# Optimization experiments

Measured on AMD Instinct MI355X. Metric: run time of the kernel, lower is better.

## Reference

```python
import jax, jax.numpy as jnp
import numpy as np

B, N, K, C = 2, 2048, 48, 128
FF = 4 * C
EPS = 1e-5
SCALE = 30.0

def _gelu(x):
    return jax.nn.gelu(x, approximate=False)

def _ln(x, g, b):
    m = jnp.mean(x, axis=-1, keepdims=True)
    v = jnp.var(x, axis=-1, keepdims=True)
    return g * (x - m) * jax.lax.rsqrt(v + EPS) + b

def _gather_nodes(nodes, idx):
    # nodes [B,N,C], idx [B,N,K] -> [B,N,K,C]
    return jnp.take_along_axis(nodes[:, :, None, :], idx[..., None], axis=1)

def setup_inputs() -> dict:
    key = jax.random.key(0)
    ks = jax.random.split(key, 16)
    def w(k, i, o):
        return (jax.random.normal(k, (i, o), jnp.float32) / np.sqrt(i)).astype(jnp.float32)
    inp = {
        'h_V': jax.random.normal(ks[0], (B, N, C), jnp.float32),
        'h_E': jax.random.normal(ks[1], (B, N, K, C), jnp.float32),
        'E_idx': jax.random.randint(ks[2], (B, N, K), 0, N),
        'mask_V': jnp.ones((B, N), jnp.float32),
        'mask_attend': jnp.ones((B, N, K), jnp.float32),
        'W1_w': w(ks[3], 3 * C, C), 'W1_b': jnp.zeros((C,), jnp.float32),
        'W2_w': w(ks[4], C, C), 'W2_b': jnp.zeros((C,), jnp.float32),
        'W3_w': w(ks[5], C, C), 'W3_b': jnp.zeros((C,), jnp.float32),
        'W11_w': w(ks[6], 3 * C, C), 'W11_b': jnp.zeros((C,), jnp.float32),
        'W12_w': w(ks[7], C, C), 'W12_b': jnp.zeros((C,), jnp.float32),
        'W13_w': w(ks[8], C, C), 'W13_b': jnp.zeros((C,), jnp.float32),
        'Win_w': w(ks[9], C, FF), 'Win_b': jnp.zeros((FF,), jnp.float32),
        'Wout_w': w(ks[10], FF, C), 'Wout_b': jnp.zeros((C,), jnp.float32),
        'g1': jnp.ones((C,), jnp.float32), 'b1': jnp.zeros((C,), jnp.float32),
        'g2': jnp.ones((C,), jnp.float32), 'b2': jnp.zeros((C,), jnp.float32),
        'g3': jnp.ones((C,), jnp.float32), 'b3': jnp.zeros((C,), jnp.float32),
    }
    return inp

def _edge_mlp(h_V, h_E, E_idx, Wa_w, Wa_b, Wb_w, Wb_b, Wc_w, Wc_b):
    h_nbr = _gather_nodes(h_V, E_idx)                       # [B,N,K,C]
    h_ctr = jnp.broadcast_to(h_V[:, :, None, :], h_nbr.shape)
    h_EV = jnp.concatenate([h_ctr, h_E, h_nbr], axis=-1)   # [B,N,K,3C]
    h = _gelu(h_EV @ Wa_w + Wa_b)
    h = _gelu(h @ Wb_w + Wb_b)
    return h @ Wc_w + Wc_b                                  # [B,N,K,C]

def reference(h_V, h_E, E_idx, mask_V, mask_attend,
              W1_w, W1_b, W2_w, W2_b, W3_w, W3_b,
              W11_w, W11_b, W12_w, W12_b, W13_w, W13_b,
              Win_w, Win_b, Wout_w, Wout_b,
              g1, b1, g2, b2, g3, b3):
    # message pass on nodes
    h_msg = _edge_mlp(h_V, h_E, E_idx, W1_w, W1_b, W2_w, W2_b, W3_w, W3_b)
    h_msg = mask_attend[..., None] * h_msg
    dh = jnp.sum(h_msg, axis=-2) / SCALE
    h_V = _ln(h_V + dh, g1, b1)
    # position-wise FFN
    dh = _gelu(h_V @ Win_w + Win_b) @ Wout_w + Wout_b
    h_V = _ln(h_V + dh, g2, b2)
    h_V = mask_V[..., None] * h_V
    # edge update
    h_msg = _edge_mlp(h_V, h_E, E_idx, W11_w, W11_b, W12_w, W12_b, W13_w, W13_b)
    h_E = _ln(h_E + h_msg, g3, b3)
    return (h_V, h_E)
```

## Files before the change

### kernel.cpp

```cpp
#include <hip/hip_runtime.h>
#include <hip/hip_bf16.h>

#define BB 2
#define NN 2048
#define KE 48
#define CC 128
#define FFD 512
#define K3 384

typedef short sx8 __attribute__((ext_vector_type(8)));
typedef float fx4 __attribute__((ext_vector_type(4)));

__device__ __forceinline__ short f2bs(float f) {
    __bf16 h = (__bf16)f;
    return __builtin_bit_cast(short, h);
}

__device__ __forceinline__ float gelu_f(float x) {
    float z = fabsf(x) * 0.70710678118654752f;
    float e = __expf(-z * z);
    float t = __builtin_amdgcn_rcpf(fmaf(0.3275911f, z, 1.0f));
    float poly = t * fmaf(t, fmaf(t, fmaf(t, fmaf(t, 1.061405429f, -1.453152027f),
                                          1.421413741f), -0.284496736f), 0.254829592f);
    float erf = 1.0f - poly * e;
    float phi = fmaf(copysignf(erf, x), 0.5f, 0.5f);
    return x * phi;
}

__device__ __forceinline__ sx8 cvt8f(const float* p) {
    float4 a = *(const float4*)p;
    float4 b = *(const float4*)(p + 4);
    sx8 r;
    r[0] = f2bs(a.x); r[1] = f2bs(a.y); r[2] = f2bs(a.z); r[3] = f2bs(a.w);
    r[4] = f2bs(b.x); r[5] = f2bs(b.y); r[6] = f2bs(b.z); r[7] = f2bs(b.w);
    return r;
}

__device__ __forceinline__ sx8 pack8(float4 a, float4 b) {
    sx8 r;
    r[0] = f2bs(a.x); r[1] = f2bs(a.y); r[2] = f2bs(a.z); r[3] = f2bs(a.w);
    r[4] = f2bs(b.x); r[5] = f2bs(b.y); r[6] = f2bs(b.z); r[7] = f2bs(b.w);
    return r;
}

__global__ void prep_weights(const float* __restrict__ W1, const float* __restrict__ W2,
                             const float* __restrict__ W3, const float* __restrict__ W11,
                             const float* __restrict__ W12, const float* __restrict__ W13,
                             const float* __restrict__ Win, const float* __restrict__ Wout,
                             short* __restrict__ wt) {
    int i = blockIdx.x * 256 + threadIdx.x;
    const float* src;
    short* dst;
    int R, S, local;
    if (i < 49152)       { src = W1;   dst = wt;          R = 384; S = 128; local = i; }
    else if (i < 65536)  { src = W2;   dst = wt + 49152;  R = 128; S = 128; local = i - 49152; }
    else if (i < 81920)  { src = W3;   dst = wt + 65536;  R = 128; S = 128; local = i - 65536; }
    else if (i < 131072) { src = W11;  dst = wt + 81920;  R = 384; S = 128; local = i - 81920; }
    else if (i < 147456) { src = W12;  dst = wt + 131072; R = 128; S = 128; local = i - 131072; }
    else if (i < 163840) { src = W13;  dst = wt + 147456; R = 128; S = 128; local = i - 147456; }
    else if (i < 229376) { src = Win;  dst = wt + 163840; R = 128; S = 512; local = i - 163840; }
    else                 { src = Wout; dst = wt + 229376; R = 512; S = 128; local = i - 229376; }
    int c = local / R;
    int r = local - c * R;
    dst[local] = f2bs(src[r * S + c]);
}

template <int PASS>
__global__ __launch_bounds__(256, 5) void edge_pass(
    const float* __restrict__ hVsrc, const float* __restrict__ hE,
    const int* __restrict__ Eidx,
    const short* __restrict__ WaT, const float* __restrict__ Wab,
    const short* __restrict__ WbT, const float* __restrict__ Wbb,
    const short* __restrict__ WcT, const float* __restrict__ Wcb,
    const float* __restrict__ mask_att, float* __restrict__ hv1_out,
    const float* __restrict__ gamma, const float* __restrict__ beta,
    float* __restrict__ hE_out) {
    __shared__ __align__(16) unsigned char smem_raw[48 * 264 * 2];

    short* A0   = (short*)smem_raw;
    short* Xs   = (short*)smem_raw;
    float* S    = (float*)smem_raw;
    float* dhp  = (float*)(smem_raw + 13056);
    float* redp = (float*)(smem_raw + 15104);

    const int tid = threadIdx.x;
    const int bn  = blockIdx.x;
    const int bb  = bn >> 11;
    const int wave = tid >> 6, lane = tid & 63, q = lane >> 4, m16 = lane & 15;
    const int col0 = wave * 32 + m16;
    const int col1 = col0 + 16;
    const int r0 = tid >> 4, seg = tid & 15;

    const int e0 = Eidx[bn * KE + r0];
    const int e1 = Eidx[bn * KE + r0 + 16];
    const int e2 = Eidx[bn * KE + r0 + 32];

    {
        const float* he  = hE + (size_t)bn * KE * CC + seg * 8;
        float4 h0a = *(const float4*)(he + r0 * CC);
        float4 h0b = *(const float4*)(he + r0 * CC + 4);
        float4 h1a = *(const float4*)(he + (r0 + 16) * CC);
        float4 h1b = *(const float4*)(he + (r0 + 16) * CC + 4);
        float4 h2a = *(const float4*)(he + (r0 + 32) * CC);
        float4 h2b = *(const float4*)(he + (r0 + 32) * CC + 4);
        *(sx8*)(A0 + r0 * 264 + seg * 8)        = pack8(h0a, h0b);
        *(sx8*)(A0 + (r0 + 16) * 264 + seg * 8) = pack8(h1a, h1b);
        *(sx8*)(A0 + (r0 + 32) * 264 + seg * 8) = pack8(h2a, h2b);
    }
    {
        const float* hvb = hVsrc + (size_t)bb * NN * CC + seg * 8;
        float4 n0a = *(const float4*)(hvb + (size_t)e0 * CC);
        float4 n0b = *(const float4*)(hvb + (size_t)e0 * CC + 4);
        float4 n1a = *(const float4*)(hvb + (size_t)e1 * CC);
        float4 n1b = *(const float4*)(hvb + (size_t)e1 * CC + 4);
        float4 n2a = *(const float4*)(hvb + (size_t)e2 * CC);
        float4 n2b = *(const float4*)(hvb + (size_t)e2 * CC + 4);
        *(sx8*)(A0 + r0 * 264 + 128 + seg * 8)        = pack8(n0a, n0b);
        *(sx8*)(A0 + (r0 + 16) * 264 + 128 + seg * 8) = pack8(n1a, n1b);
        *(sx8*)(A0 + (r0 + 32) * 264 + 128 + seg * 8) = pack8(n2a, n2b);
    }

    const float* ctr = hVsrc + (size_t)bn * CC;
    fx4 acc[3][2];
    {
        sx8 cA[4], s0f[4], s1f[4];
#pragma unroll
        for (int kk = 0; kk < 4; ++kk) {
            cA[kk]  = cvt8f(ctr + kk * 32 + q * 8);
            s0f[kk] = *(const sx8*)(WaT + col0 * K3 + kk * 32 + q * 8);
            s1f[kk] = *(const sx8*)(WaT + col1 * K3 + kk * 32 + q * 8);
        }
        fx4 c0, c1;
#pragma unroll
        for (int r = 0; r < 4; ++r) { c0[r] = 0.0f; c1[r] = 0.0f; }
#pragma unroll
        for (int kk = 0; kk < 4; ++kk) {
            c0 = __builtin_amdgcn_mfma_f32_16x16x32_bf16(cA[kk], s0f[kk], c0, 0, 0, 0);
            c1 = __builtin_amdgcn_mfma_f32_16x16x32_bf16(cA[kk], s1f[kk], c1, 0, 0, 0);
        }
#pragma unroll
        for (int mt = 0; mt < 3; ++mt) { acc[mt][0] = c0; acc[mt][1] = c1; }
    }

    sx8 b0[4], b1[4];
#pragma unroll
    for (int kk = 0; kk < 4; ++kk) {
        b0[kk] = *(const sx8*)(WaT + col0 * K3 + 128 + kk * 32 + q * 8);
        b1[kk] = *(const sx8*)(WaT + col1 * K3 + 128 + kk * 32 + q * 8);
    }
    __syncthreads();

#pragma unroll
    for (int half = 0; half < 2; ++half) {
        if (half) {
#pragma unroll
            for (int kk = 0; kk < 4; ++kk) {
                b0[kk] = *(const sx8*)(WaT + col0 * K3 + 256 + kk * 32 + q * 8);
                b1[kk] = *(const sx8*)(WaT + col1 * K3 + 256 + kk * 32 + q * 8);
            }
        }
#pragma unroll
        for (int kk = 0; kk < 4; ++kk) {
#pragma unroll
            for (int mt = 0; mt < 3; ++mt) {
                sx8 af = *(const sx8*)(A0 + (mt * 16 + m16) * 264 + half * 128 + kk * 32 + q * 8);
                acc[mt][0] = __builtin_amdgcn_mfma_f32_16x16x32_bf16(af, b0[kk], acc[mt][0], 0, 0, 0);
                acc[mt][1] = __builtin_amdgcn_mfma_f32_16x16x32_bf16(af, b1[kk], acc[mt][1], 0, 0, 0);
            }
        }
    }

    sx8 p0[4], p1[4];
#pragma unroll
    for (int kk = 0; kk < 4; ++kk) {
        p0[kk] = *(const sx8*)(WbT + col0 * CC + kk * 32 + q * 8);
        p1[kk] = *(const sx8*)(WbT + col1 * CC + kk * 32 + q * 8);
    }
    __syncthreads();

    {
        float ba0 = Wab[col0], ba1 = Wab[col1];
#pragma unroll
        for (int mt = 0; mt < 3; ++mt)
#pragma unroll
            for (int r = 0; r < 4; ++r) {
                int row = mt * 16 + q * 4 + r;
                Xs[row * 136 + col0] = f2bs(gelu_f(acc[mt][0][r] + ba0));
                Xs[row * 136 + col1] = f2bs(gelu_f(acc[mt][1][r] + ba1));
            }
    }
    __syncthreads();

    fx4 acc2[3][2];
#pragma unroll
    for (int mt = 0; mt < 3; ++mt)
#pragma unroll
        for (int nt = 0; nt < 2; ++nt)
#pragma unroll
            for (int r = 0; r < 4; ++r) acc2[mt][nt][r] = 0.0f;
#pragma unroll
    for (int kk = 0; kk < 4; ++kk) {
#pragma unroll
        for (int mt = 0; mt < 3; ++mt) {
            sx8 af = *(const sx8*)(Xs + (mt * 16 + m16) * 136 + kk * 32 + q * 8);
            acc2[mt][0] = __builtin_amdgcn_mfma_f32_16x16x32_bf16(af, p0[kk], acc2[mt][0], 0, 0, 0);
            acc2[mt][1] = __builtin_amdgcn_mfma_f32_16x16x32_bf16(af, p1[kk], acc2[mt][1], 0, 0, 0);
        }
    }

    sx8 t0[4], t1[4];
#pragma unroll
    for (int kk = 0; kk < 4; ++kk) {
        t0[kk] = *(const sx8*)(WcT + col0 * CC + kk * 32 + q * 8);
        t1[kk] = *(const sx8*)(WcT + col1 * CC + kk * 32 + q * 8);
    }
    float mrow[12];
    float res0[12], res1[12];
    if constexpr (PASS == 1) {
#pragma unroll
        for (int mt = 0; mt < 3; ++mt)
#pragma unroll
            for (int r = 0; r < 4; ++r)
                mrow[mt * 4 + r] = mask_att[bn * KE + mt * 16 + q * 4 + r];
    } else {
#pragma unroll
        for (int mt = 0; mt < 3; ++mt)
#pragma unroll
            for (int r = 0; r < 4; ++r) {
                int row = mt * 16 + q * 4 + r;
                res0[mt * 4 + r] = hE[((size_t)bn * KE + row) * CC + col0];
                res1[mt * 4 + r] = hE[((size_t)bn * KE + row) * CC + col1];
            }
    }
    __syncthreads();

    {
        float bb0 = Wbb[col0], bb1 = Wbb[col1];
#pragma unroll
        for (int mt = 0; mt < 3; ++mt)
#pragma unroll
            for (int r = 0; r < 4; ++r) {
                int row = mt * 16 + q * 4 + r;
                Xs[row * 136 + col0] = f2bs(gelu_f(acc2[mt][0][r] + bb0));
                Xs[row * 136 + col1] = f2bs(gelu_f(acc2[mt][1][r] + bb1));
            }
    }
    __syncthreads();

    fx4 acc3[3][2];
#pragma unroll
    for (int mt = 0; mt < 3; ++mt)
#pragma unroll
        for (int nt = 0; nt < 2; ++nt)
#pragma unroll
            for (int r = 0; r < 4; ++r) acc3[mt][nt][r] = 0.0f;
#pragma unroll
    for (int kk = 0; kk < 4; ++kk) {
#pragma unroll
        for (int mt = 0; mt < 3; ++mt) {
            sx8 af = *(const sx8*)(Xs + (mt * 16 + m16) * 136 + kk * 32 + q * 8);
            acc3[mt][0] = __builtin_amdgcn_mfma_f32_16x16x32_bf16(af, t0[kk], acc3[mt][0], 0, 0, 0);
            acc3[mt][1] = __builtin_amdgcn_mfma_f32_16x16x32_bf16(af, t1[kk], acc3[mt][1], 0, 0, 0);
        }
    }

    float bc0 = Wcb[col0], bc1 = Wcb[col1];

    if constexpr (PASS == 1) {
        float ps0 = 0.f, ps1 = 0.f;
#pragma unroll
        for (int mt = 0; mt < 3; ++mt)
#pragma unroll
            for (int r = 0; r < 4; ++r) {
                float m = mrow[mt * 4 + r];
                ps0 += m * (acc3[mt][0][r] + bc0);
                ps1 += m * (acc3[mt][1][r] + bc1);
            }
        dhp[q * 128 + col0] = ps0;
        dhp[q * 128 + col1] = ps1;
        __syncthreads();
        float val = 0.f;
        if (tid < 128) {
            float dh = dhp[tid] + dhp[128 + tid] + dhp[256 + tid] + dhp[384 + tid];
            val = hVsrc[(size_t)bn * CC + tid] + dh * (1.0f / 30.0f);
            float sv1 = val, sv2 = val * val;
#pragma unroll
            for (int m = 32; m >= 1; m >>= 1) {
                sv1 += __shfl_xor(sv1, m);
                sv2 += __shfl_xor(sv2, m);
            }
            if ((tid & 63) == 0) {
                redp[(tid >> 6) * 2]     = sv1;
                redp[(tid >> 6) * 2 + 1] = sv2;
            }
        }
        __syncthreads();
        if (tid < 128) {
            float mean = (redp[0] + redp[2]) * (1.0f / 128.0f);
            float var  = (redp[1] + redp[3]) * (1.0f / 128.0f) - mean * mean;
            float rstd = rsqrtf(fmaxf(var, 0.0f) + 1e-5f);
            hv1_out[(size_t)bn * CC + tid] = gamma[tid] * (val - mean) * rstd + beta[tid];
        }
    } else {
        __syncthreads();
#pragma unroll
        for (int mt = 0; mt < 3; ++mt)
#pragma unroll
            for (int r = 0; r < 4; ++r) {
                int row = mt * 16 + q * 4 + r;
                S[row * 132 + col0] = res0[mt * 4 + r] + acc3[mt][0][r] + bc0;
                S[row * 132 + col1] = res1[mt * 4 + r] + acc3[mt][1][r] + bc1;
            }
        __syncthreads();
        int g = tid >> 5, l32 = tid & 31;
        for (int r = g; r < 48; r += 8) {
            float x0 = S[r * 132 + l32];
            float x1 = S[r * 132 + l32 + 32];
            float x2 = S[r * 132 + l32 + 64];
            float x3 = S[r * 132 + l32 + 96];
            float sv1 = x0 + x1 + x2 + x3;
            float sv2 = x0 * x0 + x1 * x1 + x2 * x2 + x3 * x3;
#pragma unroll
            for (int m = 16; m >= 1; m >>= 1) {
                sv1 += __shfl_xor(sv1, m, 32);
                sv2 += __shfl_xor(sv2, m, 32);
            }
            float mean = sv1 * (1.0f / 128.0f);
            float var  = sv2 * (1.0f / 128.0f) - mean * mean;
            float rstd = rsqrtf(fmaxf(var, 0.0f) + 1e-5f);
            float* orow = hE_out + ((size_t)bn * KE + r) * CC;
            orow[l32]      = gamma[l32] * (x0 - mean) * rstd + beta[l32];
            orow[l32 + 32] = gamma[l32 + 32] * (x1 - mean) * rstd + beta[l32 + 32];
            orow[l32 + 64] = gamma[l32 + 64] * (x2 - mean) * rstd + beta[l32 + 64];
            orow[l32 + 96] = gamma[l32 + 96] * (x3 - mean) * rstd + beta[l32 + 96];
        }
    }
}

__global__ __launch_bounds__(256, 1) void ffn_kernel(
    float* __restrict__ hv, const short* __restrict__ WinT,
    const float* __restrict__ Winb, const short* __restrict__ WoutT,
    const float* __restrict__ Woutb, const float* __restrict__ g2,
    const float* __restrict__ b2, const float* __restrict__ maskV) {
    __shared__ __align__(16) float hvF[16 * 132];
    __shared__ __align__(16) short Abf[16 * 136];
    __shared__ __align__(16) short Xs[16 * 520];

    const int tid = threadIdx.x;
    const int bn  = blockIdx.x;
    const int wave = tid >> 6, lane = tid & 63, q = lane >> 4, m16 = lane & 15;
    const int col0 = wave * 32 + m16, col1 = col0 + 16;

    sx8 bw[4][8];
#pragma unroll
    for (int kk = 0; kk < 4; ++kk)
#pragma unroll
        for (int nt = 0; nt < 8; ++nt)
            bw[kk][nt] = *(const sx8*)(WinT + (wave * 128 + nt * 16 + m16) * CC + kk * 32 + q * 8);

    for (int i = tid; i < 512; i += 256) {
        int row = i >> 5;
        int c4  = (i & 31) * 4;
        float4 v = *(const float4*)(hv + (bn * 16 + row) * CC + c4);
        hvF[row * 132 + c4]     = v.x;
        hvF[row * 132 + c4 + 1] = v.y;
        hvF[row * 132 + c4 + 2] = v.z;
        hvF[row * 132 + c4 + 3] = v.w;
        Abf[row * 136 + c4]     = f2bs(v.x);
        Abf[row * 136 + c4 + 1] = f2bs(v.y);
        Abf[row * 136 + c4 + 2] = f2bs(v.z);
        Abf[row * 136 + c4 + 3] = f2bs(v.w);
    }
    __syncthreads();

    fx4 acc1[8];
#pragma unroll
    for (int nt = 0; nt < 8; ++nt)
#pragma unroll
        for (int r = 0; r < 4; ++r) acc1[nt][r] = 0.0f;

#pragma unroll
    for (int kk = 0; kk < 4; ++kk) {
        sx8 af = *(const sx8*)(Abf + m16 * 136 + kk * 32 + q * 8);
#pragma unroll
        for (int nt = 0; nt < 8; ++nt)
            acc1[nt] = __builtin_amdgcn_mfma_f32_16x16x32_bf16(af, bw[kk][nt], acc1[nt], 0, 0, 0);
    }

    sx8 c0a[16], c1a[16];
#pragma unroll
    for (int kk = 0; kk < 16; ++kk) {
        c0a[kk] = *(const sx8*)(WoutT + col0 * FFD + kk * 32 + q * 8);
        c1a[kk] = *(const sx8*)(WoutT + col1 * FFD + kk * 32 + q * 8);
    }

#pragma unroll
    for (int nt = 0; nt < 8; ++nt) {
        int coln = wave * 128 + nt * 16 + m16;
        float bi = Winb[coln];
#pragma unroll
        for (int r = 0; r < 4; ++r) {
            int row = q * 4 + r;
            Xs[row * 520 + coln] = f2bs(gelu_f(acc1[nt][r] + bi));
        }
    }
    __syncthreads();

    fx4 o0, o1;
#pragma unroll
    for (int r = 0; r < 4; ++r) { o0[r] = 0.0f; o1[r] = 0.0f; }
#pragma unroll
    for (int kk = 0; kk < 16; ++kk) {
        sx8 af = *(const sx8*)(Xs + m16 * 520 + kk * 32 + q * 8);
        o0 = __builtin_amdgcn_mfma_f32_16x16x32_bf16(af, c0a[kk], o0, 0, 0, 0);
        o1 = __builtin_amdgcn_mfma_f32_16x16x32_bf16(af, c1a[kk], o1, 0, 0, 0);
    }
    {
        float bo0 = Woutb[col0], bo1 = Woutb[col1];
#pragma unroll
        for (int r = 0; r < 4; ++r) {
            int row = q * 4 + r;
            hvF[row * 132 + col0] += o0[r] + bo0;
            hvF[row * 132 + col1] += o1[r] + bo1;
        }
    }
    __syncthreads();

    int g = tid >> 5, l32 = tid & 31;
#pragma unroll
    for (int rr = 0; rr < 2; ++rr) {
        int row = g + rr * 8;
        float x0 = hvF[row * 132 + l32];
        float x1 = hvF[row * 132 + l32 + 32];
        float x2 = hvF[row * 132 + l32 + 64];
        float x3 = hvF[row * 132 + l32 + 96];
        float s1 = x0 + x1 + x2 + x3;
        float s2 = x0 * x0 + x1 * x1 + x2 * x2 + x3 * x3;
#pragma unroll
        for (int m = 16; m >= 1; m >>= 1) {
            s1 += __shfl_xor(s1, m, 32);
            s2 += __shfl_xor(s2, m, 32);
        }
        float mean = s1 * (1.0f / 128.0f);
        float var  = s2 * (1.0f / 128.0f) - mean * mean;
        float rstd = rsqrtf(fmaxf(var, 0.0f) + 1e-5f);
        int node = bn * 16 + row;
        float mk = maskV[node];
        float* orow = hv + node * CC;
        orow[l32]      = mk * (g2[l32] * (x0 - mean) * rstd + b2[l32]);
        orow[l32 + 32] = mk * (g2[l32 + 32] * (x1 - mean) * rstd + b2[l32 + 32]);
        orow[l32 + 64] = mk * (g2[l32 + 64] * (x2 - mean) * rstd + b2[l32 + 64]);
        orow[l32 + 96] = mk * (g2[l32 + 96] * (x3 - mean) * rstd + b2[l32 + 96]);
    }
}

extern "C" void kernel_launch(void* const* d_in, const int* in_sizes, int n_in,
                              void* d_out, int out_size, void* d_ws, size_t ws_size,
                              hipStream_t stream) {
    (void)in_sizes; (void)n_in; (void)out_size; (void)ws_size;
    const float* hV    = (const float*)d_in[0];
    const float* hE    = (const float*)d_in[1];
    const int*   Eidx  = (const int*)d_in[2];
    const float* maskV = (const float*)d_in[3];
    const float* maskA = (const float*)d_in[4];
    const float* W1w  = (const float*)d_in[5];
    const float* W1b  = (const float*)d_in[6];
    const float* W2w  = (const float*)d_in[7];
    const float* W2b  = (const float*)d_in[8];
    const float* W3w  = (const float*)d_in[9];
    const float* W3b  = (const float*)d_in[10];
    const float* W11w = (const float*)d_in[11];
    const float* W11b = (const float*)d_in[12];
    const float* W12w = (const float*)d_in[13];
    const float* W12b = (const float*)d_in[14];
    const float* W13w = (const float*)d_in[15];
    const float* W13b = (const float*)d_in[16];
    const float* Winw = (const float*)d_in[17];
    const float* Winb = (const float*)d_in[18];
    const float* Woutw = (const float*)d_in[19];
    const float* Woutb = (const float*)d_in[20];
    const float* g1 = (const float*)d_in[21];
    const float* b1 = (const float*)d_in[22];
    const float* g2 = (const float*)d_in[23];
    const float* b2 = (const float*)d_in[24];
    const float* g3 = (const float*)d_in[25];
    const float* b3 = (const float*)d_in[26];

    short* wt   = (short*)d_ws;
    float* outV = (float*)d_out;
    float* outE = outV + (size_t)BB * NN * CC;

    prep_weights<<<1152, 256, 0, stream>>>(W1w, W2w, W3w, W11w, W12w, W13w, Winw, Woutw, wt);
    edge_pass<1><<<BB * NN, 256, 0, stream>>>(hV, hE, Eidx,
                                              wt, W1b, wt + 49152, W2b, wt + 65536, W3b,
                                              maskA, outV, g1, b1, nullptr);
    ffn_kernel<<<256, 256, 0, stream>>>(outV, wt + 163840, Winb, wt + 229376, Woutb, g2, b2, maskV);
    edge_pass<2><<<BB * NN, 256, 0, stream>>>(outV, hE, Eidx,
                                              wt + 81920, W11b, wt + 131072, W12b, wt + 147456, W13b,
                                              nullptr, nullptr, g3, b3, outE);
}
```

Measured before the change: 395.0 us.

## Precompute per-node center and neighbor projections of first edge layer

The first edge-MLP layer is split by linearity. The center and neighbor parts of W·[h_ctr,h_E,h_nbr] are computed once per node in a new precompute kernel, yielding Pc and Pn. The edge kernel then gathers the Pn rows for each neighbor and only runs the h_E third of the matmul, which cuts first-layer MFMA work to a third and shrinks shared memory. The cost is two extra launches, an fp32 scratch buffer, and scattered per-element gathers of Pn in place of coalesced row loads.

```diff
diff --git a/kernel.cpp b/kernel.cpp
--- a/kernel.cpp
+++ b/kernel.cpp
@@ -65,17 +65,61 @@
     dst[local] = f2bs(src[r * S + c]);
 }
 
+__global__ __launch_bounds__(256) void precompute_P(
+    const float* __restrict__ hv, const short* __restrict__ WT,
+    const float* __restrict__ bias, float* __restrict__ Pc,
+    float* __restrict__ Pn) {
+    __shared__ __align__(16) short Abf[16 * 136];
+    const int tid = threadIdx.x;
+    const int bn  = blockIdx.x;
+    const int wave = tid >> 6, lane = tid & 63, q = lane >> 4, m16 = lane & 15;
+    const int col0 = wave * 32 + m16, col1 = col0 + 16;
+
+    {
+        int row = tid >> 4, seg = tid & 15;
+        Abf[row * 136 + seg * 8 + 0] = 0;
+        *(sx8*)(Abf + row * 136 + seg * 8) = cvt8f(hv + (size_t)(bn * 16 + row) * CC + seg * 8);
+    }
+    __syncthreads();
+
+    fx4 c0, c1, n0, n1;
+#pragma unroll
+    for (int r = 0; r < 4; ++r) { c0[r] = 0.f; c1[r] = 0.f; n0[r] = 0.f; n1[r] = 0.f; }
+#pragma unroll
+    for (int kk = 0; kk < 4; ++kk) {
+        sx8 af = *(const sx8*)(Abf + m16 * 136 + kk * 32 + q * 8);
+        sx8 bc0 = *(const sx8*)(WT + col0 * K3 + kk * 32 + q * 8);
+        sx8 bc1 = *(const sx8*)(WT + col1 * K3 + kk * 32 + q * 8);
+        sx8 bn0 = *(const sx8*)(WT + col0 * K3 + 256 + kk * 32 + q * 8);
+        sx8 bn1 = *(const sx8*)(WT + col1 * K3 + 256 + kk * 32 + q * 8);
+        c0 = __builtin_amdgcn_mfma_f32_16x16x32_bf16(af, bc0, c0, 0, 0, 0);
+        c1 = __builtin_amdgcn_mfma_f32_16x16x32_bf16(af, bc1, c1, 0, 0, 0);
+        n0 = __builtin_amdgcn_mfma_f32_16x16x32_bf16(af, bn0, n0, 0, 0, 0);
+        n1 = __builtin_amdgcn_mfma_f32_16x16x32_bf16(af, bn1, n1, 0, 0, 0);
+    }
+    float bi0 = bias[col0], bi1 = bias[col1];
+#pragma unroll
+    for (int r = 0; r < 4; ++r) {
+        int node = bn * 16 + q * 4 + r;
+        Pc[(size_t)node * CC + col0] = c0[r] + bi0;
+        Pc[(size_t)node * CC + col1] = c1[r] + bi1;
+        Pn[(size_t)node * CC + col0] = n0[r];
+        Pn[(size_t)node * CC + col1] = n1[r];
+    }
+}
+
 template <int PASS>
 __global__ __launch_bounds__(256, 5) void edge_pass(
     const float* __restrict__ hVsrc, const float* __restrict__ hE,
     const int* __restrict__ Eidx,
-    const short* __restrict__ WaT, const float* __restrict__ Wab,
+    const short* __restrict__ WaT,
     const short* __restrict__ WbT, const float* __restrict__ Wbb,
     const short* __restrict__ WcT, const float* __restrict__ Wcb,
+    const float* __restrict__ Pc, const float* __restrict__ Pn,
     const float* __restrict__ mask_att, float* __restrict__ hv1_out,
     const float* __restrict__ gamma, const float* __restrict__ beta,
     float* __restrict__ hE_out) {
-    __shared__ __align__(16) unsigned char smem_raw[48 * 264 * 2];
+    __shared__ __align__(16) unsigned char smem_raw[PASS == 1 ? 15120 : 25344];
 
     short* A0   = (short*)smem_raw;
     short* Xs   = (short*)smem_raw;
@@ -91,55 +135,36 @@
     const int col1 = col0 + 16;
     const int r0 = tid >> 4, seg = tid & 15;
 
-    const int e0 = Eidx[bn * KE + r0];
-    const int e1 = Eidx[bn * KE + r0 + 16];
-    const int e2 = Eidx[bn * KE + r0 + 32];
+    int e[3][4];
+#pragma unroll
+    for (int mt = 0; mt < 3; ++mt)
+#pragma unroll
+        for (int r = 0; r < 4; ++r)
+            e[mt][r] = Eidx[bn * KE + mt * 16 + q * 4 + r];
+
+    float pc0 = Pc[(size_t)bn * CC + col0];
+    float pc1 = Pc[(size_t)bn * CC + col1];
+    float pn0[3][4], pn1[3][4];
+#pragma unroll
+    for (int mt = 0; mt < 3; ++mt)
+#pragma unroll
+        for (int r = 0; r < 4; ++r) {
+            size_t prow = ((size_t)bb * NN + e[mt][r]) * CC;
+            pn0[mt][r] = Pn[prow + col0];
+            pn1[mt][r] = Pn[prow + col1];
+        }
 
     {
-        const float* he  = hE + (size_t)bn * KE * CC + seg * 8;
+        const float* he = hE + (size_t)bn * KE * CC + seg * 8;
         float4 h0a = *(const float4*)(he + r0 * CC);
         float4 h0b = *(const float4*)(he + r0 * CC + 4);
         float4 h1a = *(const float4*)(he + (r0 + 16) * CC);
         float4 h1b = *(const float4*)(he + (r0 + 16) * CC + 4);
         float4 h2a = *(const float4*)(he + (r0 + 32) * CC);
         float4 h2b = *(const float4*)(he + (r0 + 32) * CC + 4);
-        *(sx8*)(A0 + r0 * 264 + seg * 8)        = pack8(h0a, h0b);
-        *(sx8*)(A0 + (r0 + 16) * 264 + seg * 8) = pack8(h1a, h1b);
-        *(sx8*)(A0 + (r0 + 32) * 264 + seg * 8) = pack8(h2a, h2b);
-    }
-    {
-        const float* hvb = hVsrc + (size_t)bb * NN * CC + seg * 8;
-        float4 n0a = *(const float4*)(hvb + (size_t)e0 * CC);
-        float4 n0b = *(const float4*)(hvb + (size_t)e0 * CC + 4);
-        float4 n1a = *(const float4*)(hvb + (size_t)e1 * CC);
-        float4 n1b = *(const float4*)(hvb + (size_t)e1 * CC + 4);
-        float4 n2a = *(const float4*)(hvb + (size_t)e2 * CC);
-        float4 n2b = *(const float4*)(hvb + (size_t)e2 * CC + 4);
-        *(sx8*)(A0 + r0 * 264 + 128 + seg * 8)        = pack8(n0a, n0b);
-        *(sx8*)(A0 + (r0 + 16) * 264 + 128 + seg * 8) = pack8(n1a, n1b);
-        *(sx8*)(A0 + (r0 + 32) * 264 + 128 + seg * 8) = pack8(n2a, n2b);
-    }
-
-    const float* ctr = hVsrc + (size_t)bn * CC;
-    fx4 acc[3][2];
-    {
-        sx8 cA[4], s0f[4], s1f[4];
-#pragma unroll
-        for (int kk = 0; kk < 4; ++kk) {
-            cA[kk]  = cvt8f(ctr + kk * 32 + q * 8);
-            s0f[kk] = *(const sx8*)(WaT + col0 * K3 + kk * 32 + q * 8);
-            s1f[kk] = *(const sx8*)(WaT + col1 * K3 + kk * 32 + q * 8);
-        }
-        fx4 c0, c1;
-#pragma unroll
-        for (int r = 0; r < 4; ++r) { c0[r] = 0.0f; c1[r] = 0.0f; }
-#pragma unroll
-        for (int kk = 0; kk < 4; ++kk) {
-            c0 = __builtin_amdgcn_mfma_f32_16x16x32_bf16(cA[kk], s0f[kk], c0, 0, 0, 0);
-            c1 = __builtin_amdgcn_mfma_f32_16x16x32_bf16(cA[kk], s1f[kk], c1, 0, 0, 0);
-        }
-#pragma unroll
-        for (int mt = 0; mt < 3; ++mt) { acc[mt][0] = c0; acc[mt][1] = c1; }
+        *(sx8*)(A0 + r0 * 136 + seg * 8)        = pack8(h0a, h0b);
+        *(sx8*)(A0 + (r0 + 16) * 136 + seg * 8) = pack8(h1a, h1b);
+        *(sx8*)(A0 + (r0 + 32) * 136 + seg * 8) = pack8(h2a, h2b);
     }
 
     sx8 b0[4], b1[4];
@@ -150,23 +175,20 @@
     }
     __syncthreads();
 
-#pragma unroll
-    for (int half = 0; half < 2; ++half) {
-        if (half) {
-#pragma unroll
-            for (int kk = 0; kk < 4; ++kk) {
-                b0[kk] = *(const sx8*)(WaT + col0 * K3 + 256 + kk * 32 + q * 8);
-                b1[kk] = *(const sx8*)(WaT + col1 * K3 + 256 + kk * 32 + q * 8);
-            }
-        }
-#pragma unroll
-        for (int kk = 0; kk < 4; ++kk) {
-#pragma unroll
-            for (int mt = 0; mt < 3; ++mt) {
-                sx8 af = *(const sx8*)(A0 + (mt * 16 + m16) * 264 + half * 128 + kk * 32 + q * 8);
-                acc[mt][0] = __builtin_amdgcn_mfma_f32_16x16x32_bf16(af, b0[kk], acc[mt][0], 0, 0, 0);
-                acc[mt][1] = __builtin_amdgcn_mfma_f32_16x16x32_bf16(af, b1[kk], acc[mt][1], 0, 0, 0);
-            }
+    fx4 acc[3][2];
+#pragma unroll
+    for (int mt = 0; mt < 3; ++mt)
+#pragma unroll
+        for (int nt = 0; nt < 2; ++nt)
+#pragma unroll
+            for (int r = 0; r < 4; ++r) acc[mt][nt][r] = 0.0f;
+#pragma unroll
+    for (int kk = 0; kk < 4; ++kk) {
+#pragma unroll
+        for (int mt = 0; mt < 3; ++mt) {
+            sx8 af = *(const sx8*)(A0 + (mt * 16 + m16) * 136 + kk * 32 + q * 8);
+            acc[mt][0] = __builtin_amdgcn_mfma_f32_16x16x32_bf16(af, b0[kk], acc[mt][0], 0, 0, 0);
+            acc[mt][1] = __builtin_amdgcn_mfma_f32_16x16x32_bf16(af, b1[kk], acc[mt][1], 0, 0, 0);
         }
     }
 
@@ -178,17 +200,14 @@
     }
     __syncthreads();
 
-    {
-        float ba0 = Wab[col0], ba1 = Wab[col1];
-#pragma unroll
-        for (int mt = 0; mt < 3; ++mt)
-#pragma unroll
-            for (int r = 0; r < 4; ++r) {
-                int row = mt * 16 + q * 4 + r;
-                Xs[row * 136 + col0] = f2bs(gelu_f(acc[mt][0][r] + ba0));
-                Xs[row * 136 + col1] = f2bs(gelu_f(acc[mt][1][r] + ba1));
-            }
-    }
+#pragma unroll
+    for (int mt = 0; mt < 3; ++mt)
+#pragma unroll
+        for (int r = 0; r < 4; ++r) {
+            int row = mt * 16 + q * 4 + r;
+            Xs[row * 136 + col0] = f2bs(gelu_f(acc[mt][0][r] + pc0 + pn0[mt][r]));
+            Xs[row * 136 + col1] = f2bs(gelu_f(acc[mt][1][r] + pc1 + pn1[mt][r]));
+        }
     __syncthreads();
 
     fx4 acc2[3][2];
@@ -487,15 +506,19 @@
     const float* b3 = (const float*)d_in[26];
 
     short* wt   = (short*)d_ws;
+    float* Pc   = (float*)((char*)d_ws + 589824);
+    float* Pn   = Pc + (size_t)BB * NN * CC;
     float* outV = (float*)d_out;
     float* outE = outV + (size_t)BB * NN * CC;
 
     prep_weights<<<1152, 256, 0, stream>>>(W1w, W2w, W3w, W11w, W12w, W13w, Winw, Woutw, wt);
+    precompute_P<<<256, 256, 0, stream>>>(hV, wt, W1b, Pc, Pn);
     edge_pass<1><<<BB * NN, 256, 0, stream>>>(hV, hE, Eidx,
-                                              wt, W1b, wt + 49152, W2b, wt + 65536, W3b,
-                                              maskA, outV, g1, b1, nullptr);
+                                              wt, wt + 49152, W2b, wt + 65536, W3b,
+                                              Pc, Pn, maskA, outV, g1, b1, nullptr);
     ffn_kernel<<<256, 256, 0, stream>>>(outV, wt + 163840, Winb, wt + 229376, Woutb, g2, b2, maskV);
+    precompute_P<<<256, 256, 0, stream>>>(outV, wt + 81920, W11b, Pc, Pn);
     edge_pass<2><<<BB * NN, 256, 0, stream>>>(outV, hE, Eidx,
-                                              wt + 81920, W11b, wt + 131072, W12b, wt + 147456, W13b,
-                                              nullptr, nullptr, g3, b3, outE);
-}
+                                              wt + 81920, wt + 131072, W12b, wt + 147456, W13b,
+                                              Pc, Pn, nullptr, nullptr, g3, b3, outE);
+}
```

Result: faster. 348.9 us (-11.7%).
